# Kernel optimization log

Measured on AMD Instinct MI355X. Metric: run time of the kernel, lower is better.

Reference implementation:

```python
import jax, jax.numpy as jnp
import numpy as np

N_NODES = 100000
N_EDGES = 1600000
D_IN = 128
D_HID = 128


def gcn_conv(x, src, dst, deg_inv_sqrt, W, b, n_nodes):
    """GCNConv: out = D^{-1/2}(A+I)D^{-1/2} (x @ W) + b.

    src/dst already include self-loops; deg_inv_sqrt precomputed per node.
    """
    h = x @ W  # [N, D_out]
    coef = deg_inv_sqrt[src] * deg_inv_sqrt[dst]  # [E+N]
    msg = h[src] * coef[:, None]  # [E+N, D_out] -- dominant memory traffic
    out = jax.ops.segment_sum(msg, dst, num_segments=n_nodes)
    return out + b


def reference(x, edge_index, W1, b1, W2, b2):
    n_nodes = x.shape[0]
    loop = jnp.arange(n_nodes, dtype=edge_index.dtype)
    src = jnp.concatenate([edge_index[0], loop])
    dst = jnp.concatenate([edge_index[1], loop])
    deg = jax.ops.segment_sum(jnp.ones_like(src, dtype=x.dtype), dst,
                              num_segments=n_nodes)
    deg_inv_sqrt = jnp.where(deg > 0, jax.lax.rsqrt(jnp.maximum(deg, 1.0)), 0.0)

    h = gcn_conv(x, src, dst, deg_inv_sqrt, W1, b1, n_nodes)
    h = jax.nn.relu(h)
    h = gcn_conv(h, src, dst, deg_inv_sqrt, W2, b2, n_nodes)
    return h.mean(axis=0)  # [D_HID]


def setup_inputs() -> dict:
    key = jax.random.key(0)
    k1, k2, k3, k4, k5 = jax.random.split(key, 5)
    x = jax.random.normal(k1, (N_NODES, D_IN), dtype=jnp.float32)
    edge_index = jax.random.randint(k2, (2, N_EDGES), 0, N_NODES, dtype=jnp.int64)
    s1 = 1.0 / np.sqrt(D_IN)
    s2 = 1.0 / np.sqrt(D_HID)
    W1 = jax.random.uniform(k3, (D_IN, D_HID), jnp.float32, -s1, s1)
    W2 = jax.random.uniform(k4, (D_HID, D_HID), jnp.float32, -s2, s2)
    b1 = jnp.zeros((D_HID,), jnp.float32)
    b2 = jnp.zeros((D_HID,), jnp.float32)
    return {"x": x, "edge_index": edge_index, "W1": W1, "b1": b1,
            "W2": W2, "b2": b2}
```

## Files before the change

kernel.cpp:

```cpp
#include <hip/hip_runtime.h>

#define NN 100000
#define NE 1600000
#define DD 128
#define BSH 8
#define NB 391
#define CAP 4608
#define SSH 9
#define NBS 196
#define CAP2 9472
#define NAB 6250
#define NRB 125

typedef float f32x2 __attribute__((ext_vector_type(2)));
typedef float f32x4 __attribute__((ext_vector_type(4)));
typedef short s16x8 __attribute__((ext_vector_type(8)));

static __device__ __forceinline__ unsigned short f2bf(float f) {
    unsigned u = __float_as_uint(f);
    return (unsigned short)((u + 0x7fffu + ((u >> 16) & 1u)) >> 16);
}


__global__ __launch_bounds__(256) void k_part(const int* __restrict__ src, const int* __restrict__ dst,
                                              int* __restrict__ bcursor, int* __restrict__ bcursor2,
                                              unsigned* __restrict__ part, unsigned* __restrict__ part2) {
    __shared__ int histD[NB], rankD[NB], bblD[NB];
    __shared__ int histS[NBS], rankS[NBS], bblS[NBS];
    int t = threadIdx.x;
    for (int j = t; j < NB; j += 256) histD[j] = 0;
    if (t < NBS) histS[t] = 0;
    __syncthreads();
    int base = blockIdx.x * 4096;
    int s[16], d[16];
    #pragma unroll
    for (int j = 0; j < 16; j++) {
        int i = base + j * 256 + t;
        if (i < NE) {
            s[j] = src[i]; d[j] = dst[i];
            atomicAdd(&histD[d[j] >> BSH], 1);
            atomicAdd(&histS[s[j] >> SSH], 1);
        } else d[j] = -1;
    }
    __syncthreads();
    for (int j = t; j < NB; j += 256) { bblD[j] = atomicAdd(&bcursor[j], histD[j]);  rankD[j] = 0; }
    if (t < NBS) { bblS[t] = atomicAdd(&bcursor2[t], histS[t]); rankS[t] = 0; }
    __syncthreads();
    #pragma unroll
    for (int j = 0; j < 16; j++) {
        if (d[j] >= 0) {
            int bD = d[j] >> BSH;
            int r = bblD[bD] + atomicAdd(&rankD[bD], 1);
            if (r < CAP)
                part[(size_t)bD * CAP + r] = (unsigned)s[j] | ((unsigned)(d[j] & 255) << 17);
            int bS = s[j] >> SSH;
            int r2 = bblS[bS] + atomicAdd(&rankS[bS], 1);
            if (r2 < CAP2)
                part2[(size_t)bS * CAP2 + r2] = (unsigned)d[j] | ((unsigned)(s[j] & 511) << 17);
        }
    }
}


__global__ __launch_bounds__(256) void k_csr(const unsigned* __restrict__ part, const int* __restrict__ bcursor,
                                             int* __restrict__ offs, int* __restrict__ oend,
                                             float* __restrict__ dis, int* __restrict__ csr,
                                             unsigned* __restrict__ hs) {
    __shared__ int cnt[256], offl[256], s2[256];
    int t = threadIdx.x;
    int b = blockIdx.x;
    if (b == 0 && t < 32) hs[(unsigned)NN * 32u + t] = 0u;
    int dlo = b << BSH;
    int nn_b = NN - dlo; if (nn_b > 256) nn_b = 256;
    int c = bcursor[b]; if (c > CAP) c = CAP;
    size_t e0 = (size_t)b * CAP;
    cnt[t] = 0;
    __syncthreads();
    for (int i = t; i < c; i += 256)
        atomicAdd(&cnt[part[e0 + i] >> 17], 1);
    __syncthreads();
    int a = cnt[t];
    s2[t] = a;
    __syncthreads();
    for (int off = 1; off < 256; off <<= 1) {
        int add = (t >= off) ? s2[t - off] : 0;
        __syncthreads();
        s2[t] += add;
        __syncthreads();
    }
    int ex = s2[t] - a;
    offl[t] = ex;
    if (t < nn_b) {
        offs[dlo + t] = (int)e0 + ex;
        oend[dlo + t] = (int)e0 + ex + a;
        dis[dlo + t] = rsqrtf((float)a + 1.0f);
    }
    cnt[t] = 0;
    __syncthreads();
    for (int i = t; i < c; i += 256) {
        unsigned e = part[e0 + i];
        int li = (int)(e >> 17);
        int p = (int)e0 + offl[li] + atomicAdd(&cnt[li], 1);
        csr[p] = (int)(e & 0x1FFFFu);
    }
}


__global__ __launch_bounds__(256) void k_coefb(const unsigned* __restrict__ part2, const int* __restrict__ bcursor2,
                                               const float* __restrict__ dis, float* __restrict__ coef) {
    __shared__ float accL[512];
    int t = threadIdx.x;
    int b = blockIdx.x;
    int dlo = b << SSH;
    int nn_b = NN - dlo; if (nn_b > 512) nn_b = 512;
    int c = bcursor2[b]; if (c > CAP2) c = CAP2;
    size_t e0 = (size_t)b * CAP2;
    accL[t] = 0.f; accL[t + 256] = 0.f;
    __syncthreads();
    for (int i = t; i < c; i += 256) {
        unsigned e = part2[e0 + i];
        atomicAdd(&accL[e >> 17], dis[e & 0x1FFFFu]);
    }
    __syncthreads();
    #pragma unroll
    for (int q = 0; q < 2; q++) {
        int i = t + q * 256;
        if (i < nn_b) coef[dlo + i] = accL[i];
    }
}


__global__ __launch_bounds__(256) void k_gemm(const float* __restrict__ Ap, const float* __restrict__ W,
                                              const float* __restrict__ dis, unsigned* __restrict__ hs) {
    __shared__ unsigned WF[8192];
    int tid = threadIdx.x;
    #pragma unroll
    for (int i = 0; i < 32; i++) {
        int e = i * 256 + tid;
        int jw = e & 3, lane = (e >> 2) & 63, kk = (e >> 8) & 3, nt = e >> 10;
        int r0 = kk * 32 + ((lane >> 4) << 3) + (jw << 1);
        int c = (nt << 4) + (lane & 15);
        unsigned lo = f2bf(W[r0 * DD + c]);
        unsigned hi = f2bf(W[(r0 + 1) * DD + c]);
        WF[e] = lo | (hi << 16);
    }

    int lane = tid & 63;
    int w = tid >> 6;
    int rowBase = blockIdx.x * 128 + w * 32;
    int lg = lane >> 4;
    int ll = lane & 15;

    s16x8 af[2][4];
    #pragma unroll
    for (int mt = 0; mt < 2; mt++) {
        int r = rowBase + mt * 16 + ll;
        if (r >= NN) r = NN - 1;
        const char* xp = (const char*)Ap + ((unsigned)r * 512u + (unsigned)lg * 32u);
        #pragma unroll
        for (int kk = 0; kk < 4; kk++) {
            f32x4 a0 = *(const f32x4*)(xp + kk * 128);
            f32x4 a1 = *(const f32x4*)(xp + kk * 128 + 16);
            s16x8 tt;
            tt[0] = (short)f2bf(a0[0]); tt[1] = (short)f2bf(a0[1]);
            tt[2] = (short)f2bf(a0[2]); tt[3] = (short)f2bf(a0[3]);
            tt[4] = (short)f2bf(a1[0]); tt[5] = (short)f2bf(a1[1]);
            tt[6] = (short)f2bf(a1[2]); tt[7] = (short)f2bf(a1[3]);
            af[mt][kk] = tt;
        }
    }
    __syncthreads();

    f32x4 acc[2][8];
    #pragma unroll
    for (int m = 0; m < 2; m++)
        #pragma unroll
        for (int n = 0; n < 8; n++) acc[m][n] = (f32x4){0.f, 0.f, 0.f, 0.f};

    const s16x8* wfrag = (const s16x8*)WF;

    #pragma unroll
    for (int kk = 0; kk < 4; kk++) {
        #pragma unroll
        for (int nt = 0; nt < 8; nt++) {
            s16x8 bf = wfrag[(nt * 4 + kk) * 64 + lane];
            acc[0][nt] = __builtin_amdgcn_mfma_f32_16x16x32_bf16(bf, af[0][kk], acc[0][nt], 0, 0, 0);
            acc[1][nt] = __builtin_amdgcn_mfma_f32_16x16x32_bf16(bf, af[1][kk], acc[1][nt], 0, 0, 0);
        }
    }

    #pragma unroll
    for (int mt = 0; mt < 2; mt++) {
        int grow = rowBase + mt * 16 + ll;
        if (grow < NN) {
            float dn = dis[grow];
            unsigned* orow = (unsigned*)((char*)hs + ((unsigned)grow * 128u));
            #pragma unroll
            for (int nt = 0; nt < 8; nt++) {
                f32x4 v = acc[mt][nt];
                int u = 0;
                u = __builtin_amdgcn_cvt_pk_fp8_f32(v[0] * dn, v[1] * dn, u, false);
                u = __builtin_amdgcn_cvt_pk_fp8_f32(v[2] * dn, v[3] * dn, u, true);
                orow[nt * 4 + lg] = (unsigned)u;
            }
        }
    }
}


__global__ __launch_bounds__(256) void k_agg1(const unsigned* __restrict__ hs4, const float* __restrict__ dis,
                                              const int* __restrict__ offs, const int* __restrict__ oend,
                                              const int* __restrict__ csr, const float* __restrict__ bias,
                                              const float* __restrict__ coef, float* __restrict__ partials) {
    __shared__ float red[4][DD];
    int lane = threadIdx.x & 63;
    int half = lane >> 5;
    int li = lane & 31;
    int wv = threadIdx.x >> 6;
    int node0 = (blockIdx.x * 4 + wv) * 4;
    unsigned li4 = (unsigned)li << 2;
    const char* hb = (const char*)hs4;
    f32x2 v01 = {0.f, 0.f}, v23 = {0.f, 0.f};
    f32x4 bv = *(const f32x4*)&bias[li * 4];

    #pragma unroll 1
    for (int q = 0; q < 4; q++) {
        int node = node0 + q;
        int beg = offs[node], end = oend[node];
        float dn = dis[node];
        f32x2 a01 = {0.f, 0.f}, a23 = {0.f, 0.f};

        int s[8];
        {
            int idx = beg + half * 8;
            #pragma unroll
            for (int j = 0; j < 8; j++) s[j] = (idx + j < end) ? csr[idx + j] : NN;
        }
        #pragma unroll 1
        for (int i = beg; i < end; i += 16) {
            unsigned r[8];
            #pragma unroll
            for (int j = 0; j < 8; j++)
                r[j] = *(const unsigned*)(hb + (((unsigned)s[j] << 7) + li4));
            int nidx = i + 16 + half * 8;
            int ns[8];
            #pragma unroll
            for (int j = 0; j < 8; j++) ns[j] = (nidx + j < end) ? csr[nidx + j] : NN;
            #pragma unroll
            for (int j = 0; j < 8; j++) {
                a01 += __builtin_amdgcn_cvt_pk_f32_fp8(r[j], false);
                a23 += __builtin_amdgcn_cvt_pk_f32_fp8(r[j], true);
            }
            #pragma unroll
            for (int j = 0; j < 8; j++) s[j] = ns[j];
        }

        a01[0] += __shfl_xor(a01[0], 32);
        a01[1] += __shfl_xor(a01[1], 32);
        a23[0] += __shfl_xor(a23[0], 32);
        a23[1] += __shfl_xor(a23[1], 32);

        if (half == 0) {
            unsigned su = *(const unsigned*)(hb + (((unsigned)node << 7) + li4));
            f32x2 sl = __builtin_amdgcn_cvt_pk_f32_fp8(su, false);
            f32x2 sh = __builtin_amdgcn_cvt_pk_f32_fp8(su, true);
            float o0 = fmaxf(dn * (a01[0] + sl[0]) + bv[0], 0.f);
            float o1 = fmaxf(dn * (a01[1] + sl[1]) + bv[1], 0.f);
            float o2 = fmaxf(dn * (a23[0] + sh[0]) + bv[2], 0.f);
            float o3 = fmaxf(dn * (a23[1] + sh[1]) + bv[3], 0.f);
            float wt = (coef[node] + dn) * dn;
            v01[0] += wt * o0; v01[1] += wt * o1;
            v23[0] += wt * o2; v23[1] += wt * o3;
        }
    }

    if (half == 0) {
        red[wv][li * 4 + 0] = v01[0];
        red[wv][li * 4 + 1] = v01[1];
        red[wv][li * 4 + 2] = v23[0];
        red[wv][li * 4 + 3] = v23[1];
    }
    __syncthreads();
    int t = threadIdx.x;
    if (t < DD)
        partials[(size_t)blockIdx.x * DD + t] = red[0][t] + red[1][t] + red[2][t] + red[3][t];
}


__global__ __launch_bounds__(128) void k_red1(const float* __restrict__ partials, float* __restrict__ s1) {
    int t = threadIdx.x, b = blockIdx.x;
    float s = 0.f;
    for (int r = b * 50; r < b * 50 + 50; r++) s += partials[(size_t)r * DD + t];
    s1[b * DD + t] = s;
}

__global__ __launch_bounds__(128) void k_out(const float* __restrict__ s1, const float* __restrict__ W2,
                                             const float* __restrict__ b2, float* __restrict__ out) {
    __shared__ float v[DD];
    int t = threadIdx.x;
    float s = 0.f;
    for (int r = 0; r < NRB; r++) s += s1[r * DD + t];
    v[t] = s * (1.0f / NN);
    __syncthreads();
    float o = b2[t];
    for (int k = 0; k < DD; k++) o += v[k] * W2[k * DD + t];
    out[t] = o;
}


extern "C" void kernel_launch(void* const* d_in, const int* in_sizes, int n_in,
                              void* d_out, int out_size, void* d_ws, size_t ws_size,
                              hipStream_t stream) {
    const float* x  = (const float*)d_in[0];
    const int*   ei = (const int*)d_in[1];
    const float* W1 = (const float*)d_in[2];
    const float* b1 = (const float*)d_in[3];
    const float* W2 = (const float*)d_in[4];
    const float* b2 = (const float*)d_in[5];
    float* out = (float*)d_out;
    const int* esrc = ei;
    const int* edst = ei + NE;

    char* p = (char*)d_ws;
    unsigned* part  = (unsigned*)p;      p += (size_t)NB * CAP * 4;
    unsigned* part2 = (unsigned*)p;      p += (size_t)NBS * CAP2 * 4;
    int* csr       = (int*)p;            p += (size_t)NB * CAP * 4;
    int* offs      = (int*)p;            p += (((size_t)NN * 4) + 255) & ~(size_t)255;
    int* oend      = (int*)p;            p += (((size_t)NN * 4) + 255) & ~(size_t)255;
    float* dis     = (float*)p;          p += (((size_t)NN * 4) + 255) & ~(size_t)255;
    float* coef    = (float*)p;          p += (((size_t)NN * 4) + 255) & ~(size_t)255;
    int* bcursor   = (int*)p;            p += (((size_t)(NB + NBS) * 4) + 255) & ~(size_t)255;
    unsigned* hs   = (unsigned*)p;       p += (size_t)(NN + 1) * DD;
    float* partials = (float*)p;         p += (size_t)NAB * DD * 4;
    float* s1      = (float*)p;          p += (size_t)NRB * DD * 4;
    int* bcursor2  = bcursor + NB;

    hipMemsetAsync(bcursor, 0, (NB + NBS) * 4, stream);

    k_part<<<(NE + 4095) / 4096, 256, 0, stream>>>(esrc, edst, bcursor, bcursor2, part, part2);
    k_csr<<<NB, 256, 0, stream>>>(part, bcursor, offs, oend, dis, csr, hs);
    k_coefb<<<NBS, 256, 0, stream>>>(part2, bcursor2, dis, coef);

    k_gemm<<<(NN + 127) / 128, 256, 0, stream>>>(x, W1, dis, hs);
    k_agg1<<<NAB, 256, 0, stream>>>(hs, dis, offs, oend, csr, b1, coef, partials);

    k_red1<<<NRB, 128, 0, stream>>>(partials, s1);
    k_out<<<1, 128, 0, stream>>>(s1, W2, b2, out);
}
```

Baseline: 153.0 us.

## Pad CSR neighbor lists to multiples of 16 and use vector index loads

Each node's CSR segment is padded to a multiple of 16 entries, with the padding filled by a sentinel index pointing at a zero row. The aggregation loop can then read indices with aligned 128-bit loads and drop the per-element bounds checks and the software prefetch of the next batch of indices. In exchange the CSR buffer grows, the CSR build kernel does extra padding writes, and the loop no longer overlaps index loads for the next batch with the current gathers.

```diff
diff --git a/kernel.cpp b/kernel.cpp
--- a/kernel.cpp
+++ b/kernel.cpp
@@ -6,6 +6,7 @@
 #define BSH 8
 #define NB 391
 #define CAP 4608
+#define CAPP 8704
 #define SSH 9
 #define NBS 196
 #define CAP2 9472
@@ -74,13 +75,15 @@
     int nn_b = NN - dlo; if (nn_b > 256) nn_b = 256;
     int c = bcursor[b]; if (c > CAP) c = CAP;
     size_t e0 = (size_t)b * CAP;
+    int e0p = b * CAPP;
     cnt[t] = 0;
     __syncthreads();
     for (int i = t; i < c; i += 256)
         atomicAdd(&cnt[part[e0 + i] >> 17], 1);
     __syncthreads();
     int a = cnt[t];
-    s2[t] = a;
+    int ap = (a + 15) & ~15;
+    s2[t] = ap;
     __syncthreads();
     for (int off = 1; off < 256; off <<= 1) {
         int add = (t >= off) ? s2[t - off] : 0;
@@ -88,11 +91,11 @@
         s2[t] += add;
         __syncthreads();
     }
-    int ex = s2[t] - a;
+    int ex = s2[t] - ap;
     offl[t] = ex;
     if (t < nn_b) {
-        offs[dlo + t] = (int)e0 + ex;
-        oend[dlo + t] = (int)e0 + ex + a;
+        offs[dlo + t] = e0p + ex;
+        oend[dlo + t] = e0p + ex + ap;
         dis[dlo + t] = rsqrtf((float)a + 1.0f);
     }
     cnt[t] = 0;
@@ -100,8 +103,13 @@
     for (int i = t; i < c; i += 256) {
         unsigned e = part[e0 + i];
         int li = (int)(e >> 17);
-        int p = (int)e0 + offl[li] + atomicAdd(&cnt[li], 1);
+        int p = e0p + offl[li] + atomicAdd(&cnt[li], 1);
         csr[p] = (int)(e & 0x1FFFFu);
+    }
+    __syncthreads();
+    if (t < nn_b) {
+        int base2 = e0p + offl[t];
+        for (int i = a; i < ap; i++) csr[base2 + i] = NN;
     }
 }
 
@@ -226,33 +234,29 @@
     #pragma unroll 1
     for (int q = 0; q < 4; q++) {
         int node = node0 + q;
-        int beg = offs[node], end = oend[node];
+        int beg = offs[node], endp = oend[node];
         float dn = dis[node];
         f32x2 a01 = {0.f, 0.f}, a23 = {0.f, 0.f};
 
-        int s[8];
-        {
-            int idx = beg + half * 8;
-            #pragma unroll
-            for (int j = 0; j < 8; j++) s[j] = (idx + j < end) ? csr[idx + j] : NN;
-        }
         #pragma unroll 1
-        for (int i = beg; i < end; i += 16) {
+        for (int i = beg; i < endp; i += 16) {
+            const int* cp = csr + i + half * 8;
+            int4 sa = *(const int4*)cp;
+            int4 sb = *(const int4*)(cp + 4);
             unsigned r[8];
-            #pragma unroll
-            for (int j = 0; j < 8; j++)
-                r[j] = *(const unsigned*)(hb + (((unsigned)s[j] << 7) + li4));
-            int nidx = i + 16 + half * 8;
-            int ns[8];
-            #pragma unroll
-            for (int j = 0; j < 8; j++) ns[j] = (nidx + j < end) ? csr[nidx + j] : NN;
+            r[0] = *(const unsigned*)(hb + (((unsigned)sa.x << 7) + li4));
+            r[1] = *(const unsigned*)(hb + (((unsigned)sa.y << 7) + li4));
+            r[2] = *(const unsigned*)(hb + (((unsigned)sa.z << 7) + li4));
+            r[3] = *(const unsigned*)(hb + (((unsigned)sa.w << 7) + li4));
+            r[4] = *(const unsigned*)(hb + (((unsigned)sb.x << 7) + li4));
+            r[5] = *(const unsigned*)(hb + (((unsigned)sb.y << 7) + li4));
+            r[6] = *(const unsigned*)(hb + (((unsigned)sb.z << 7) + li4));
+            r[7] = *(const unsigned*)(hb + (((unsigned)sb.w << 7) + li4));
             #pragma unroll
             for (int j = 0; j < 8; j++) {
                 a01 += __builtin_amdgcn_cvt_pk_f32_fp8(r[j], false);
                 a23 += __builtin_amdgcn_cvt_pk_f32_fp8(r[j], true);
             }
-            #pragma unroll
-            for (int j = 0; j < 8; j++) s[j] = ns[j];
         }
 
         a01[0] += __shfl_xor(a01[0], 32);
@@ -324,7 +328,7 @@
     char* p = (char*)d_ws;
     unsigned* part  = (unsigned*)p;      p += (size_t)NB * CAP * 4;
     unsigned* part2 = (unsigned*)p;      p += (size_t)NBS * CAP2 * 4;
-    int* csr       = (int*)p;            p += (size_t)NB * CAP * 4;
+    int* csr       = (int*)p;            p += (size_t)NB * CAPP * 4;
     int* offs      = (int*)p;            p += (((size_t)NN * 4) + 255) & ~(size_t)255;
     int* oend      = (int*)p;            p += (((size_t)NN * 4) + 255) & ~(size_t)255;
     float* dis     = (float*)p;          p += (((size_t)NN * 4) + 255) & ~(size_t)255;
```

After: 153.2 us. No clear change (+0.1%).
